# Optimization experiments

Hardware: AMD Instinct MI355X
Metric: run time of the kernel (lower is better)

The kernel has to match this reference:

```python
import jax, jax.numpy as jnp
import numpy as np

BITS = 4
N_PACK = 32 // BITS  # 8
GROUPSIZE = 128
IN_FEATURES = 4096
OUT_FEATURES = 4096


def setup_inputs() -> dict:
    key = jax.random.key(0)
    k1, k2, k3, k4 = jax.random.split(key, 4)
    x = jax.random.normal(k1, (4, 2048, IN_FEATURES), dtype=jnp.float32)
    packed_weight = jax.random.randint(
        k2, (OUT_FEATURES, IN_FEATURES // N_PACK),
        jnp.iinfo(jnp.int32).min, jnp.iinfo(jnp.int32).max, dtype=jnp.int32)
    scale = jax.random.uniform(k3, (OUT_FEATURES, IN_FEATURES // GROUPSIZE),
                               dtype=jnp.float32, minval=0.001, maxval=0.02)
    bias = jax.random.normal(k4, (OUT_FEATURES,), dtype=jnp.float32) * 0.01
    return {"x": x, "packed_weight": packed_weight, "scale": scale, "bias": bias}


def _dequant_weight(packed_weight, scale):
    # Unpack 8 signed int4 values per int32 word (symmetric path, no zero-point).
    # Matches torch recover(): (w << (32 - bits*(n_pack - e))) >> (32 - bits)
    # with arithmetic right shift giving sign extension into int8 range [-8, 7].
    e = jnp.arange(N_PACK, dtype=jnp.int32)
    left = (32 - BITS * (N_PACK - e)).astype(jnp.int32)          # [n_pack]
    w = jnp.right_shift(
        jnp.left_shift(packed_weight[:, :, None], left[None, None, :]),
        32 - BITS)                                               # [O, P, n_pack]
    w = w.reshape(OUT_FEATURES, IN_FEATURES).astype(jnp.float32)
    # Per-group scale: in_features divisible by groupsize (no-remainder branch).
    w = (w.reshape(-1, GROUPSIZE) * scale.reshape(-1, 1)).reshape(OUT_FEATURES, IN_FEATURES)
    return w


def reference(x, packed_weight, scale, bias):
    w = _dequant_weight(packed_weight, scale)      # [O, I] fp32
    # F.linear: x @ w.T + bias
    return jnp.einsum('bsi,oi->bso', x, w) + bias
```

## Files before the change

kernel.cpp:

```cpp
#include <hip/hip_runtime.h>

typedef __bf16 bf16x4 __attribute__((ext_vector_type(4)));
typedef __bf16 bf16x8 __attribute__((ext_vector_type(8)));
typedef float  f32x4  __attribute__((ext_vector_type(4)));

#define M_DIM 8192
#define N_DIM 4096
#define K_DIM 4096

#define GLDS16(gptr, lptr)                                                     \
  __builtin_amdgcn_global_load_lds(                                            \
      (const __attribute__((address_space(1))) void*)(gptr),                   \
      (__attribute__((address_space(3))) void*)(lptr), 16, 0, 0)


__global__ __launch_bounds__(256) void dequant_w_kernel(
    const int* __restrict__ pw, const float* __restrict__ scale,
    unsigned short* __restrict__ wbf) {
  int idx = blockIdx.x * 256 + threadIdx.x;
  int o = idx >> 9;
  int p = idx & 511;
  int w = pw[idx];
  float s = scale[o * 32 + (p >> 4)];
  bf16x8 v;
#pragma unroll
  for (int e = 0; e < 8; ++e) {
    int val = (int)((unsigned)w << (4 * e)) >> 28;
    v[e] = (__bf16)((float)val * s);
  }
  *(bf16x8*)&wbf[(size_t)idx * 8] = v;
}

__global__ __launch_bounds__(256) void conv_x_kernel(
    const float* __restrict__ x, unsigned short* __restrict__ xbf) {
  size_t i = (size_t)(blockIdx.x * 256 + threadIdx.x) * 8;
  float4 a = *(const float4*)&x[i];
  float4 b = *(const float4*)&x[i + 4];
  bf16x8 v = {(__bf16)a.x, (__bf16)a.y, (__bf16)a.z, (__bf16)a.w,
              (__bf16)b.x, (__bf16)b.y, (__bf16)b.z, (__bf16)b.w};
  *(bf16x8*)&xbf[i] = v;
}


template <int QM, int QN>
__device__ __forceinline__ void mfma_quad(f32x4 (&acc)[8][4],
                                          const bf16x8 (&a)[4][2],
                                          const bf16x8 (&b)[2][2]) {
  __builtin_amdgcn_s_setprio(1);
#pragma unroll
  for (int mi = 0; mi < 4; ++mi)
#pragma unroll
    for (int ni = 0; ni < 2; ++ni)
#pragma unroll
      for (int kk = 0; kk < 2; ++kk)
        acc[QM * 4 + mi][QN * 2 + ni] =
            __builtin_amdgcn_mfma_f32_16x16x32_bf16(
                a[mi][kk], b[ni][kk], acc[QM * 4 + mi][QN * 2 + ni], 0, 0, 0);
  __builtin_amdgcn_s_setprio(0);
}

#define STAGE_A(qm_, tau_)                                                     \
  do {                                                                         \
    const int k0_ = ((tau_) & 63) * 64;                                        \
    char* const base_ = lds + ((tau_) & 1) * 32768;                            \
    const int c0_ = wave * 2, c1_ = wave * 2 + 1;                              \
    const int R0_ = (qm_) * 64 + (c0_ & 7) * 8 + (c0_ >> 3) * 128;             \
    const int R1_ = (qm_) * 64 + (c1_ & 7) * 8 + (c1_ >> 3) * 128;             \
    GLDS16(xbf + (size_t)(m0 + R0_ + rs8) * K_DIM + k0_ + cs8e,                \
           base_ + R0_ * 128);                                                 \
    GLDS16(xbf + (size_t)(m0 + R1_ + rs8) * K_DIM + k0_ + cs8e,                \
           base_ + R1_ * 128);                                                 \
  } while (0)

#define STAGE_B(qn_, tau_)                                                     \
  do {                                                                         \
    const int k0_ = ((tau_) & 63) * 64;                                        \
    char* const base_ = lds + 65536 + ((tau_) & 1) * 32768;                    \
    const int c0_ = wave * 2, c1_ = wave * 2 + 1;                              \
    const int R0_ = (qn_) * 32 + (c0_ >> 2) * 64 + (c0_ & 3) * 8;              \
    const int R1_ = (qn_) * 32 + (c1_ >> 2) * 64 + (c1_ & 3) * 8;              \
    GLDS16(wbf + (size_t)(n0 + R0_ + rs8) * K_DIM + k0_ + cs8e,                \
           base_ + R0_ * 128);                                                 \
    GLDS16(wbf + (size_t)(n0 + R1_ + rs8) * K_DIM + k0_ + cs8e,                \
           base_ + R1_ * 128);                                                 \
  } while (0)

#define READ_A(d_, qm_)                                                        \
  do {                                                                         \
    const char* pA_ = lds + (d_) * 32768 + (qm_) * 8192 + aRowOff;             \
    a[0][0] = *(const bf16x8*)(pA_ + 0 + b0);                                  \
    a[0][1] = *(const bf16x8*)(pA_ + 0 + b1);                                  \
    a[1][0] = *(const bf16x8*)(pA_ + 2048 + b0);                               \
    a[1][1] = *(const bf16x8*)(pA_ + 2048 + b1);                               \
    a[2][0] = *(const bf16x8*)(pA_ + 4096 + b0);                               \
    a[2][1] = *(const bf16x8*)(pA_ + 4096 + b1);                               \
    a[3][0] = *(const bf16x8*)(pA_ + 6144 + b0);                               \
    a[3][1] = *(const bf16x8*)(pA_ + 6144 + b1);                               \
  } while (0)

#define READ_B(d_, qn_)                                                        \
  do {                                                                         \
    const char* pB_ = lds + 65536 + (d_) * 32768 + (qn_) * 4096 + bRowOff;     \
    b[0][0] = *(const bf16x8*)(pB_ + 0 + b0);                                  \
    b[0][1] = *(const bf16x8*)(pB_ + 0 + b1);                                  \
    b[1][0] = *(const bf16x8*)(pB_ + 2048 + b0);                               \
    b[1][1] = *(const bf16x8*)(pB_ + 2048 + b1);                               \
  } while (0)

#define PH_MID                                                                 \
  do {                                                                         \
    asm volatile("" ::: "memory");                                             \
    __builtin_amdgcn_s_barrier();                                              \
    asm volatile("s_waitcnt lgkmcnt(0)" ::: "memory");                         \
  } while (0)

#define PH_END                                                                 \
  do {                                                                         \
    asm volatile("" ::: "memory");                                             \
    __builtin_amdgcn_s_barrier();                                              \
  } while (0)

#define VMW6 asm volatile("s_waitcnt vmcnt(6)" ::: "memory")

__global__ __launch_bounds__(512, 2) void gemm8_kernel(
    const unsigned short* __restrict__ xbf,
    const unsigned short* __restrict__ wbf,
    const float* __restrict__ bias, float* __restrict__ out) {
  __shared__ char lds[131072];

  int bid = blockIdx.x;
  int cpx = gridDim.x >> 3;
  int swz = (bid & 7) * cpx + (bid >> 3);
  int bm = swz >> 4;
  int bn = swz & 15;
  int m0 = bm * 256, n0 = bn * 256;

  int tid = threadIdx.x;
  int lane = tid & 63;
  int wave = tid >> 6;
  int wm = wave >> 2, wn = wave & 3;
  int lr = lane & 15, lk = lane >> 4, l7 = lane & 7;

  const int rs8 = lane >> 3;
  const int cs8e = ((lane & 7) ^ rs8) * 8;
  const int b0 = ((lk ^ l7) << 4);
  const int b1 = b0 ^ 64;
  const int aRowOff = (wm * 128 + lr) * 128;
  const int bRowOff = (wn * 64 + lr) * 128;

  f32x4 acc[8][4];
#pragma unroll
  for (int i = 0; i < 8; ++i)
#pragma unroll
    for (int jx = 0; jx < 4; ++jx) acc[i][jx] = (f32x4)0.0f;

  bf16x8 a[4][2], b[2][2];

  STAGE_A(0, 0);
  STAGE_B(1, 0);
  STAGE_A(1, 0);
  STAGE_B(0, 0);
  STAGE_A(0, 1);
  STAGE_B(1, 1);
  STAGE_A(1, 1);
  VMW6;
  asm volatile("" ::: "memory");
  __builtin_amdgcn_s_barrier();

  for (int j = 0; j < K_DIM / 128; ++j) {
    int t = 2 * j;
    READ_A(0, 0);
    READ_B(0, 0);
    STAGE_B(0, t + 1);
    PH_MID;
    mfma_quad<0, 0>(acc, a, b);
    PH_END;
    READ_B(0, 1);
    STAGE_A(0, t + 2);
    PH_MID;
    mfma_quad<0, 1>(acc, a, b);
    PH_END;
    READ_A(0, 1);
    STAGE_B(1, t + 2);
    PH_MID;
    mfma_quad<1, 1>(acc, a, b);
    PH_END;
    READ_B(0, 0);
    STAGE_A(1, t + 2);
    VMW6;
    PH_MID;
    mfma_quad<1, 0>(acc, a, b);
    PH_END;
    READ_A(1, 0);
    READ_B(1, 0);
    STAGE_B(0, t + 2);
    PH_MID;
    mfma_quad<0, 0>(acc, a, b);
    PH_END;
    READ_B(1, 1);
    STAGE_A(0, t + 3);
    PH_MID;
    mfma_quad<0, 1>(acc, a, b);
    PH_END;
    READ_A(1, 1);
    STAGE_B(1, t + 3);
    PH_MID;
    mfma_quad<1, 1>(acc, a, b);
    PH_END;
    READ_B(1, 0);
    STAGE_A(1, t + 3);
    VMW6;
    PH_MID;
    mfma_quad<1, 0>(acc, a, b);
    PH_END;
  }

  asm volatile("s_waitcnt vmcnt(0)" ::: "memory");

#pragma unroll
  for (int ng = 0; ng < 4; ++ng) {
    int col = n0 + wn * 64 + ng * 16 + lr;
    float bv = bias[col];
#pragma unroll
    for (int mg = 0; mg < 8; ++mg) {
      size_t rowb = (size_t)m0 + wm * 128 + mg * 16 + lk * 4;
#pragma unroll
      for (int r = 0; r < 4; ++r)
        out[(rowb + r) * N_DIM + col] = acc[mg][ng][r] + bv;
    }
  }
}

__global__ __launch_bounds__(256) void gemm_fused_kernel(
    const float* __restrict__ x, const int* __restrict__ pw,
    const float* __restrict__ scale, const float* __restrict__ bias,
    float* __restrict__ out) {
  __shared__ unsigned short As[128 * 64];
  __shared__ unsigned short Bs[128 * 64];
  int bid = blockIdx.x;
  int cpx = gridDim.x >> 3;
  int swz = (bid & 7) * cpx + (bid >> 3);
  int bm = swz >> 5, bn = swz & 31;
  int m0 = bm * 128, n0 = bn * 128;
  int tid = threadIdx.x;
  int lane = tid & 63;
  int wave = tid >> 6;
  int wm = wave >> 1, wn = wave & 1;
  int lr = lane & 15, lk = lane >> 4;
  f32x4 acc[4][4];
#pragma unroll
  for (int i = 0; i < 4; ++i)
#pragma unroll
    for (int jx = 0; jx < 4; ++jx) acc[i][jx] = (f32x4)0.0f;
  int tr = tid >> 4, tc = tid & 15;
  float4 ra[8];
  int4 rb;
  float sB = 0.f;
#pragma unroll
  for (int i = 0; i < 8; ++i)
    ra[i] = *(const float4*)&x[(size_t)(m0 + i * 16 + tr) * K_DIM + tc * 4];
  rb = *(const int4*)&pw[(size_t)(n0 + (tid >> 1)) * 512 + (tid & 1) * 4];
  sB = scale[(size_t)(n0 + (tid >> 1)) * 32 + 0];
  const int NT = K_DIM / 64;
  for (int t = 0; t < NT; ++t) {
#pragma unroll
    for (int i = 0; i < 8; ++i) {
      float4 v = ra[i];
      bf16x4 b4 = {(__bf16)v.x, (__bf16)v.y, (__bf16)v.z, (__bf16)v.w};
      *(bf16x4*)&As[(i * 16 + tr) * 64 + tc * 4] = b4;
    }
    {
      int n = tid >> 1, h = tid & 1;
#pragma unroll
      for (int w = 0; w < 4; ++w) {
        int word = ((const int*)&rb)[w];
        bf16x8 o;
#pragma unroll
        for (int e = 0; e < 8; ++e) {
          int val = (int)((unsigned)word << (4 * e)) >> 28;
          o[e] = (__bf16)((float)val * sB);
        }
        *(bf16x8*)&Bs[n * 64 + h * 32 + w * 8] = o;
      }
    }
    if (t + 1 < NT) {
      int k1 = (t + 1) * 64;
#pragma unroll
      for (int i = 0; i < 8; ++i)
        ra[i] = *(const float4*)&x[(size_t)(m0 + i * 16 + tr) * K_DIM + k1 +
                                   tc * 4];
      rb = *(const int4*)&pw[(size_t)(n0 + (tid >> 1)) * 512 + (k1 >> 3) +
                             (tid & 1) * 4];
      sB = scale[(size_t)(n0 + (tid >> 1)) * 32 + (k1 >> 7)];
    }
    __syncthreads();
#pragma unroll
    for (int kk = 0; kk < 2; ++kk) {
      bf16x8 af[4], bfr[4];
#pragma unroll
      for (int mi = 0; mi < 4; ++mi)
        af[mi] = *(const bf16x8*)&As[(wm * 64 + mi * 16 + lr) * 64 + kk * 32 +
                                     lk * 8];
#pragma unroll
      for (int ni = 0; ni < 4; ++ni)
        bfr[ni] = *(const bf16x8*)&Bs[(wn * 64 + ni * 16 + lr) * 64 + kk * 32 +
                                      lk * 8];
#pragma unroll
      for (int mi = 0; mi < 4; ++mi)
#pragma unroll
        for (int ni = 0; ni < 4; ++ni)
          acc[mi][ni] = __builtin_amdgcn_mfma_f32_16x16x32_bf16(
              af[mi], bfr[ni], acc[mi][ni], 0, 0, 0);
    }
    __syncthreads();
  }
#pragma unroll
  for (int ni = 0; ni < 4; ++ni) {
    int col = n0 + wn * 64 + ni * 16 + lr;
    float bv = bias[col];
#pragma unroll
    for (int mi = 0; mi < 4; ++mi) {
      int rowb = m0 + wm * 64 + mi * 16 + lk * 4;
#pragma unroll
      for (int r = 0; r < 4; ++r)
        out[(size_t)(rowb + r) * N_DIM + col] = acc[mi][ni][r] + bv;
    }
  }
}

extern "C" void kernel_launch(void* const* d_in, const int* in_sizes, int n_in,
                              void* d_out, int out_size, void* d_ws,
                              size_t ws_size, hipStream_t stream) {
  const float* x = (const float*)d_in[0];
  const int* pw = (const int*)d_in[1];
  const float* scale = (const float*)d_in[2];
  const float* bias = (const float*)d_in[3];
  float* out = (float*)d_out;

  const size_t needB = (size_t)N_DIM * K_DIM * 2;
  const size_t needA = (size_t)M_DIM * K_DIM * 2;

  if (ws_size >= needA + needB) {
    unsigned short* wbf = (unsigned short*)d_ws;
    unsigned short* xbf = (unsigned short*)((char*)d_ws + needB);
    dequant_w_kernel<<<(N_DIM * (K_DIM / 8)) / 256, 256, 0, stream>>>(pw, scale,
                                                                      wbf);
    conv_x_kernel<<<((size_t)M_DIM * K_DIM / 8) / 256, 256, 0, stream>>>(x,
                                                                         xbf);
    gemm8_kernel<<<(M_DIM / 256) * (N_DIM / 256), 512, 0, stream>>>(xbf, wbf,
                                                                    bias, out);
  } else {
    gemm_fused_kernel<<<(M_DIM / 128) * (N_DIM / 128), 256, 0, stream>>>(
        x, pw, scale, bias, out);
  }
}
```

Baseline: 456.8 us.

## Double-buffer B fragments in registers and drop explicit LDS waits in GEMM

The GEMM main loop now holds two B-fragment register sets, so the B quadrant reused by the fourth MFMA phase is kept in registers rather than re-read from LDS. The explicit lgkmcnt(0) wait after each mid-phase barrier is removed, leaving the compiler to place LDS waits and allowing more overlap of LDS reads with MFMA. Separately, the fp32-to-bf16 conversion kernel now handles 4 elements per thread instead of 8 and launches twice as many threads. The extra registers may pressure occupancy at 2 blocks/CU, and relying on compiler-inserted waits around the raw barriers is a correctness risk.

Result: no change. 451.0 us (-1.3%).

```diff
diff --git a/kernel.cpp b/kernel.cpp
--- a/kernel.cpp
+++ b/kernel.cpp
@@ -33,12 +33,10 @@
 
 __global__ __launch_bounds__(256) void conv_x_kernel(
     const float* __restrict__ x, unsigned short* __restrict__ xbf) {
-  size_t i = (size_t)(blockIdx.x * 256 + threadIdx.x) * 8;
+  size_t i = (size_t)(blockIdx.x * 256 + threadIdx.x) * 4;
   float4 a = *(const float4*)&x[i];
-  float4 b = *(const float4*)&x[i + 4];
-  bf16x8 v = {(__bf16)a.x, (__bf16)a.y, (__bf16)a.z, (__bf16)a.w,
-              (__bf16)b.x, (__bf16)b.y, (__bf16)b.z, (__bf16)b.w};
-  *(bf16x8*)&xbf[i] = v;
+  bf16x4 v = {(__bf16)a.x, (__bf16)a.y, (__bf16)a.z, (__bf16)a.w};
+  *(bf16x4*)&xbf[i] = v;
 }
 
 
@@ -98,20 +96,19 @@
     a[3][1] = *(const bf16x8*)(pA_ + 6144 + b1);                               \
   } while (0)
 
-#define READ_B(d_, qn_)                                                        \
+#define READ_B(d_, qn_, dst_)                                                  \
   do {                                                                         \
     const char* pB_ = lds + 65536 + (d_) * 32768 + (qn_) * 4096 + bRowOff;     \
-    b[0][0] = *(const bf16x8*)(pB_ + 0 + b0);                                  \
-    b[0][1] = *(const bf16x8*)(pB_ + 0 + b1);                                  \
-    b[1][0] = *(const bf16x8*)(pB_ + 2048 + b0);                               \
-    b[1][1] = *(const bf16x8*)(pB_ + 2048 + b1);                               \
+    dst_[0][0] = *(const bf16x8*)(pB_ + 0 + b0);                               \
+    dst_[0][1] = *(const bf16x8*)(pB_ + 0 + b1);                               \
+    dst_[1][0] = *(const bf16x8*)(pB_ + 2048 + b0);                            \
+    dst_[1][1] = *(const bf16x8*)(pB_ + 2048 + b1);                            \
   } while (0)
 
 #define PH_MID                                                                 \
   do {                                                                         \
     asm volatile("" ::: "memory");                                             \
     __builtin_amdgcn_s_barrier();                                              \
-    asm volatile("s_waitcnt lgkmcnt(0)" ::: "memory");                         \
   } while (0)
 
 #define PH_END                                                                 \
@@ -154,7 +151,7 @@
 #pragma unroll
     for (int jx = 0; jx < 4; ++jx) acc[i][jx] = (f32x4)0.0f;
 
-  bf16x8 a[4][2], b[2][2];
+  bf16x8 a[4][2], bq0[2][2], bq1[2][2];
 
   STAGE_A(0, 0);
   STAGE_B(1, 0);
@@ -169,49 +166,47 @@
 
   for (int j = 0; j < K_DIM / 128; ++j) {
     int t = 2 * j;
+    READ_B(0, 0, bq0);
     READ_A(0, 0);
-    READ_B(0, 0);
     STAGE_B(0, t + 1);
     PH_MID;
-    mfma_quad<0, 0>(acc, a, b);
-    PH_END;
-    READ_B(0, 1);
+    mfma_quad<0, 0>(acc, a, bq0);
+    PH_END;
+    READ_B(0, 1, bq1);
     STAGE_A(0, t + 2);
     PH_MID;
-    mfma_quad<0, 1>(acc, a, b);
+    mfma_quad<0, 1>(acc, a, bq1);
     PH_END;
     READ_A(0, 1);
     STAGE_B(1, t + 2);
     PH_MID;
-    mfma_quad<1, 1>(acc, a, b);
-    PH_END;
-    READ_B(0, 0);
+    mfma_quad<1, 1>(acc, a, bq1);
+    PH_END;
     STAGE_A(1, t + 2);
     VMW6;
     PH_MID;
-    mfma_quad<1, 0>(acc, a, b);
-    PH_END;
+    mfma_quad<1, 0>(acc, a, bq0);
+    PH_END;
+    READ_B(1, 0, bq0);
     READ_A(1, 0);
-    READ_B(1, 0);
     STAGE_B(0, t + 2);
     PH_MID;
-    mfma_quad<0, 0>(acc, a, b);
-    PH_END;
-    READ_B(1, 1);
+    mfma_quad<0, 0>(acc, a, bq0);
+    PH_END;
+    READ_B(1, 1, bq1);
     STAGE_A(0, t + 3);
     PH_MID;
-    mfma_quad<0, 1>(acc, a, b);
+    mfma_quad<0, 1>(acc, a, bq1);
     PH_END;
     READ_A(1, 1);
     STAGE_B(1, t + 3);
     PH_MID;
-    mfma_quad<1, 1>(acc, a, b);
-    PH_END;
-    READ_B(1, 0);
+    mfma_quad<1, 1>(acc, a, bq1);
+    PH_END;
     STAGE_A(1, t + 3);
     VMW6;
     PH_MID;
-    mfma_quad<1, 0>(acc, a, b);
+    mfma_quad<1, 0>(acc, a, bq0);
     PH_END;
   }
 
@@ -345,7 +340,7 @@
     unsigned short* xbf = (unsigned short*)((char*)d_ws + needB);
     dequant_w_kernel<<<(N_DIM * (K_DIM / 8)) / 256, 256, 0, stream>>>(pw, scale,
                                                                       wbf);
-    conv_x_kernel<<<((size_t)M_DIM * K_DIM / 8) / 256, 256, 0, stream>>>(x,
+    conv_x_kernel<<<((size_t)M_DIM * K_DIM / 4) / 256, 256, 0, stream>>>(x,
                                                                          xbf);
     gemm8_kernel<<<(M_DIM / 256) * (N_DIM / 256), 512, 0, stream>>>(xbf, wbf,
                                                                     bias, out);
```
